# Performance work log

Measured on AMD Instinct MI355X. Metric: run time of the kernel, lower is better.

Reference implementation:

```python
import jax, jax.numpy as jnp
import numpy as np

N, E, D, ATT = 20000, 5000, 128, 32
NUM_LAYERS = 4
LN_EPS = 1e-5
DEG_EPS = 1e-12

def setup_inputs() -> dict:
    key = jax.random.key(0)
    k1, k2, k3, k4 = jax.random.split(key, 4)
    node_embeddings = jax.random.normal(k1, (N, D), dtype=jnp.float32)
    hypergraph_matrix = (jax.random.uniform(k2, (N, E)) < 0.01).astype(jnp.float32)
    ln_gamma = jnp.ones((D,), jnp.float32)
    ln_beta = jnp.zeros((D,), jnp.float32)
    W_att = jax.random.normal(k3, (D, ATT), dtype=jnp.float32) * (1.0 / np.sqrt(D))
    b_att = jnp.zeros((ATT,), jnp.float32)
    q_att = jax.random.normal(k4, (ATT,), dtype=jnp.float32)
    return {"node_embeddings": node_embeddings, "hypergraph_matrix": hypergraph_matrix,
            "ln_gamma": ln_gamma, "ln_beta": ln_beta,
            "W_att": W_att, "b_att": b_att, "q_att": q_att}

def _layernorm(y, gamma, beta):
    mu = jnp.mean(y, axis=-1, keepdims=True)
    var = jnp.mean(jnp.square(y - mu), axis=-1, keepdims=True)
    return (y - mu) * jax.lax.rsqrt(var + LN_EPS) * gamma + beta

def reference(node_embeddings, hypergraph_matrix, ln_gamma, ln_beta, W_att, b_att, q_att):
    H = hypergraph_matrix                      # [N, E]
    dv_inv = 1.0 / jnp.maximum(jnp.sum(H, axis=1), DEG_EPS)   # [N]
    de_inv = 1.0 / jnp.maximum(jnp.sum(H, axis=0), DEG_EPS)   # [E]
    x = node_embeddings
    for _ in range(NUM_LAYERS):
        edge_mean = (H.T @ x) * de_inv[:, None]       # V->E mean, [E, D]
        node_msg = (H @ edge_mean) * dv_inv[:, None]  # E->V mean, [N, D]
        x = _layernorm(node_msg + node_embeddings, ln_gamma, ln_beta)
        # dropout(p=0.35) is identity in eval mode
    # per-edge masked mean over member nodes (vectorized segment-mean)
    M = (H > 0).astype(x.dtype)                        # [N, E]
    cnt = jnp.maximum(jnp.sum(M, axis=0), 1.0)         # [E]
    edge_out = (M.T @ x) / cnt[:, None]                # [E, D]
    # dot-product attention pooling over hyperedges
    scores = jax.nn.softmax(jnp.tanh(edge_out @ W_att + b_att) @ q_att)  # [E]
    return scores @ edge_out                           # [D]
```

## Files before the change

kernel.cpp:

```cpp
#include <hip/hip_runtime.h>
#include <hip/hip_fp16.h>
#include <math.h>

#define NN 20000
#define EE 5000
#define DD 128
#define ATT 32
#define NUM_LAYERS 4
#define LN_EPS 1e-5f
#define DEG_EPS 1e-12f

#define ECAP 320
#define NCAP 128
#define CSTRIDE 32

typedef float vfloat4 __attribute__((ext_vector_type(4)));

__device__ inline unsigned pack2h(float x, float y) {
    return __builtin_bit_cast(unsigned, __floats2half2_rn(x, y));
}
__device__ inline void acc8(float* a, uint4 u) {
    __half2 h;
    h = __builtin_bit_cast(__half2, u.x); a[0] += __low2float(h); a[1] += __high2float(h);
    h = __builtin_bit_cast(__half2, u.y); a[2] += __low2float(h); a[3] += __high2float(h);
    h = __builtin_bit_cast(__half2, u.z); a[4] += __low2float(h); a[5] += __high2float(h);
    h = __builtin_bit_cast(__half2, u.w); a[6] += __low2float(h); a[7] += __high2float(h);
}

__global__ __launch_bounds__(256) void build_adj(
    const float* __restrict__ H, int* __restrict__ cur, int* __restrict__ nc,
    int* __restrict__ el, int* __restrict__ nl) {
    const int n = blockIdx.x;
    const int tid = threadIdx.x;
    __shared__ int lcnt;
    __shared__ int lbuf[NCAP];
    if (tid == 0) lcnt = 0;
    __syncthreads();
    const vfloat4* row = reinterpret_cast<const vfloat4*>(H + (size_t)n * EE);
    for (int i = tid; i < EE / 4; i += 256) {
        const vfloat4 h = __builtin_nontemporal_load(row + i);
        float v[4] = {h.x, h.y, h.z, h.w};
        const int ebase = i * 4;
#pragma unroll
        for (int k = 0; k < 4; k++) {
            if (v[k] != 0.0f) {
                int s = atomicAdd(&lcnt, 1);
                if (s < NCAP) lbuf[s] = ebase + k;
            }
        }
    }
    __syncthreads();
    const int c = min(lcnt, NCAP);
    for (int k = tid; k < c; k += 256) {
        const int e = lbuf[k];
        nl[(size_t)n * NCAP + k] = e;
        const int slot = atomicAdd(&cur[e << 5], 1);
        if (slot < ECAP) el[(size_t)e * ECAP + slot] = n;
    }
    if (tid == 0) nc[n] = lcnt;
}

__global__ __launch_bounds__(256) void cvt_to_h(
    const float* __restrict__ src, __half* __restrict__ dst, int n4) {
    const int i = blockIdx.x * 256 + threadIdx.x;
    if (i >= n4) return;
    const float4 v = reinterpret_cast<const float4*>(src)[i];
    uint2 u; u.x = pack2h(v.x, v.y); u.y = pack2h(v.z, v.w);
    reinterpret_cast<uint2*>(dst)[i] = u;
}

template <bool FINAL>
__global__ __launch_bounds__(256) void edge_gather16(
    const __half* __restrict__ xh, const int* __restrict__ cur,
    const int* __restrict__ el, __half* __restrict__ outh,
    float* __restrict__ eout, const float* __restrict__ W,
    const float* __restrict__ bb, const float* __restrict__ qv,
    float* __restrict__ t) {
    __shared__ int ilst[ECAP];
    __shared__ float part[4][16][8];
    __shared__ float rowbuf[DD];
    const int e = blockIdx.x;
    const int tid = threadIdx.x;
    const int cnt = cur[e << 5];
    const int c = min(cnt, ECAP);
    const int* lst = el + (size_t)e * ECAP;
    for (int k = tid; k < c; k += 256) ilst[k] = lst[k];
    __syncthreads();
    const int lane16 = tid & 15;
    const int s = tid >> 4;
    const int wave = tid >> 6;
    float a[8] = {0, 0, 0, 0, 0, 0, 0, 0};
    float b[8] = {0, 0, 0, 0, 0, 0, 0, 0};
    int i = s;
    for (; i + 16 < c; i += 32) {
        const int n0 = ilst[i];
        const int n1 = ilst[i + 16];
        acc8(a, *reinterpret_cast<const uint4*>(xh + n0 * DD + lane16 * 8));
        acc8(b, *reinterpret_cast<const uint4*>(xh + n1 * DD + lane16 * 8));
    }
    if (i < c) {
        acc8(a, *reinterpret_cast<const uint4*>(xh + ilst[i] * DD + lane16 * 8));
    }
#pragma unroll
    for (int k = 0; k < 8; k++) {
        float v = a[k] + b[k];
        v += __shfl_down(v, 16);
        v += __shfl_down(v, 32);
        a[k] = v;
    }
    if ((tid & 63) < 16) {
#pragma unroll
        for (int k = 0; k < 8; k++) part[wave][lane16][k] = a[k];
    }
    __syncthreads();
    if (tid < 16) {
        const float inv = 1.0f / fmaxf((float)cnt, DEG_EPS);
        float o[8];
#pragma unroll
        for (int k = 0; k < 8; k++)
            o[k] = (part[0][tid][k] + part[1][tid][k] + part[2][tid][k] + part[3][tid][k]) * inv;
        if (!FINAL) {
            uint4 u;
            u.x = pack2h(o[0], o[1]); u.y = pack2h(o[2], o[3]);
            u.z = pack2h(o[4], o[5]); u.w = pack2h(o[6], o[7]);
            *reinterpret_cast<uint4*>(outh + e * DD + tid * 8) = u;
        } else {
#pragma unroll
            for (int k = 0; k < 8; k++) rowbuf[tid * 8 + k] = o[k];
            *reinterpret_cast<float4*>(eout + e * DD + tid * 8) =
                make_float4(o[0], o[1], o[2], o[3]);
            *reinterpret_cast<float4*>(eout + e * DD + tid * 8 + 4) =
                make_float4(o[4], o[5], o[6], o[7]);
        }
    }
    if (FINAL) {
        __syncthreads();
        float r = 0.0f;
        if (tid < ATT) {
            float acc = 0.0f;
#pragma unroll 4
            for (int d = 0; d < DD; d++) acc += rowbuf[d] * W[d * ATT + tid];
            r = tanhf(acc + bb[tid]) * qv[tid];
        }
        for (int off = 16; off > 0; off >>= 1) r += __shfl_down(r, off);
        if (tid == 0) t[e] = r;
    }
}

__global__ __launch_bounds__(128) void node_gather_ln16(
    const __half* __restrict__ emean, const int* __restrict__ nc,
    const int* __restrict__ nl, const float* __restrict__ x0,
    const float* __restrict__ gamma, const float* __restrict__ beta,
    __half* __restrict__ xout) {
    __shared__ int ilst[NCAP];
    __shared__ float part[2][16][8];
    const int n = blockIdx.x;
    const int tid = threadIdx.x;
    const int cnt = nc[n];
    const int c = min(cnt, NCAP);
    const int* lst = nl + (size_t)n * NCAP;
    if (tid < c) ilst[tid] = lst[tid];
    __syncthreads();
    const int lane16 = tid & 15;
    const int s = tid >> 4;
    const int wave = tid >> 6;
    float a[8] = {0, 0, 0, 0, 0, 0, 0, 0};
    float b[8] = {0, 0, 0, 0, 0, 0, 0, 0};
    int i = s;
    for (; i + 8 < c; i += 16) {
        const int e0 = ilst[i];
        const int e1 = ilst[i + 8];
        acc8(a, *reinterpret_cast<const uint4*>(emean + e0 * DD + lane16 * 8));
        acc8(b, *reinterpret_cast<const uint4*>(emean + e1 * DD + lane16 * 8));
    }
    if (i < c) {
        acc8(a, *reinterpret_cast<const uint4*>(emean + ilst[i] * DD + lane16 * 8));
    }
#pragma unroll
    for (int k = 0; k < 8; k++) {
        float v = a[k] + b[k];
        v += __shfl_down(v, 16);
        v += __shfl_down(v, 32);
        a[k] = v;
    }
    if ((tid & 63) < 16) {
#pragma unroll
        for (int k = 0; k < 8; k++) part[wave][lane16][k] = a[k];
    }
    __syncthreads();
    if (tid < 16) {
        const float inv = 1.0f / fmaxf((float)cnt, DEG_EPS);
        const float4 x0a = *reinterpret_cast<const float4*>(x0 + n * DD + tid * 8);
        const float4 x0b = *reinterpret_cast<const float4*>(x0 + n * DD + tid * 8 + 4);
        float y[8];
        y[0] = (part[0][tid][0] + part[1][tid][0]) * inv + x0a.x;
        y[1] = (part[0][tid][1] + part[1][tid][1]) * inv + x0a.y;
        y[2] = (part[0][tid][2] + part[1][tid][2]) * inv + x0a.z;
        y[3] = (part[0][tid][3] + part[1][tid][3]) * inv + x0a.w;
        y[4] = (part[0][tid][4] + part[1][tid][4]) * inv + x0b.x;
        y[5] = (part[0][tid][5] + part[1][tid][5]) * inv + x0b.y;
        y[6] = (part[0][tid][6] + part[1][tid][6]) * inv + x0b.z;
        y[7] = (part[0][tid][7] + part[1][tid][7]) * inv + x0b.w;
        float sm = 0.0f, ss = 0.0f;
#pragma unroll
        for (int k = 0; k < 8; k++) { sm += y[k]; ss += y[k] * y[k]; }
        for (int off = 8; off > 0; off >>= 1) {
            sm += __shfl_down(sm, off);
            ss += __shfl_down(ss, off);
        }
        sm = __shfl(sm, 0);
        ss = __shfl(ss, 0);
        const float mu = sm * (1.0f / 128.0f);
        float var = ss * (1.0f / 128.0f) - mu * mu;
        var = fmaxf(var, 0.0f);
        const float rstd = 1.0f / sqrtf(var + LN_EPS);
        const float4 g0 = *reinterpret_cast<const float4*>(gamma + tid * 8);
        const float4 g1 = *reinterpret_cast<const float4*>(gamma + tid * 8 + 4);
        const float4 b0 = *reinterpret_cast<const float4*>(beta + tid * 8);
        const float4 b1 = *reinterpret_cast<const float4*>(beta + tid * 8 + 4);
        float gg[8] = {g0.x, g0.y, g0.z, g0.w, g1.x, g1.y, g1.z, g1.w};
        float bb[8] = {b0.x, b0.y, b0.z, b0.w, b1.x, b1.y, b1.z, b1.w};
        float o[8];
#pragma unroll
        for (int k = 0; k < 8; k++) o[k] = (y[k] - mu) * rstd * gg[k] + bb[k];
        uint4 u;
        u.x = pack2h(o[0], o[1]); u.y = pack2h(o[2], o[3]);
        u.z = pack2h(o[4], o[5]); u.w = pack2h(o[6], o[7]);
        *reinterpret_cast<uint4*>(xout + n * DD + tid * 8) = u;
    }
}

__global__ __launch_bounds__(1024) void softmax_stats(
    const float* __restrict__ t, float* __restrict__ MS) {
    __shared__ float red[16];
    __shared__ float smax;
    const int tid = threadIdx.x;
    const int wid = tid >> 6;
    float m = -1e30f;
    for (int i = tid; i < EE; i += 1024) m = fmaxf(m, t[i]);
    for (int off = 32; off > 0; off >>= 1) m = fmaxf(m, __shfl_down(m, off));
    if ((tid & 63) == 0) red[wid] = m;
    __syncthreads();
    if (tid < 64) {
        float v = (tid < 16) ? red[tid] : -1e30f;
        for (int off = 8; off > 0; off >>= 1) v = fmaxf(v, __shfl_down(v, off));
        if (tid == 0) smax = v;
    }
    __syncthreads();
    const float M = smax;
    float sum = 0.0f;
    for (int i = tid; i < EE; i += 1024) sum += expf(t[i] - M);
    for (int off = 32; off > 0; off >>= 1) sum += __shfl_down(sum, off);
    if ((tid & 63) == 0) red[wid] = sum;
    __syncthreads();
    if (tid < 64) {
        float v = (tid < 16) ? red[tid] : 0.0f;
        for (int off = 8; off > 0; off >>= 1) v += __shfl_down(v, off);
        if (tid == 0) { MS[0] = M; MS[1] = v; }
    }
}

__global__ __launch_bounds__(128) void weighted_sum(
    const float* __restrict__ eout, const float* __restrict__ t,
    const float* __restrict__ MS, float* __restrict__ out) {
    const int d = threadIdx.x;
    const float M = MS[0];
    const float invS = 1.0f / MS[1];
    float acc = 0.0f;
    for (int e = blockIdx.x; e < EE; e += gridDim.x) {
        const float w = expf(t[e] - M);
        acc += w * eout[e * DD + d];
    }
    atomicAdd(&out[d], acc * invS);
}

extern "C" void kernel_launch(void* const* d_in, const int* in_sizes, int n_in,
                              void* d_out, int out_size, void* d_ws, size_t ws_size,
                              hipStream_t stream) {
    const float* x0 = (const float*)d_in[0];
    const float* H = (const float*)d_in[1];
    const float* gamma = (const float*)d_in[2];
    const float* beta = (const float*)d_in[3];
    const float* W = (const float*)d_in[4];
    const float* b = (const float*)d_in[5];
    const float* qv = (const float*)d_in[6];
    float* out = (float*)d_out;

    char* w = (char*)d_ws;
    int* cur = (int*)w;       w += (size_t)EE * CSTRIDE * 4;
    int* nc = (int*)w;        w += (size_t)NN * 4;
    int* el = (int*)w;        w += (size_t)EE * ECAP * 4;
    int* nl = (int*)w;        w += (size_t)NN * NCAP * 4;
    __half* xh0 = (__half*)w; w += (size_t)NN * DD * 2;
    __half* xA = (__half*)w;  w += (size_t)NN * DD * 2;
    __half* xB = (__half*)w;  w += (size_t)NN * DD * 2;
    __half* emean = (__half*)w; w += (size_t)EE * DD * 2;
    float* eout = (float*)w;  w += (size_t)EE * DD * 4;
    float* t = (float*)w;     w += (size_t)EE * 4;
    float* MS = (float*)w;    w += 16;

    hipMemsetAsync(cur, 0, (size_t)EE * CSTRIDE * 4, stream);
    hipMemsetAsync(d_out, 0, (size_t)DD * sizeof(float), stream);

    build_adj<<<NN, 256, 0, stream>>>(H, cur, nc, el, nl);
    cvt_to_h<<<(NN * DD / 4 + 255) / 256, 256, 0, stream>>>(x0, xh0, NN * DD / 4);

    const __half* xin = xh0;
    __half* bufs[2] = {xA, xB};
    for (int l = 0; l < NUM_LAYERS; l++) {
        edge_gather16<false><<<EE, 256, 0, stream>>>(
            xin, cur, el, emean, nullptr, nullptr, nullptr, nullptr, nullptr);
        node_gather_ln16<<<NN, 128, 0, stream>>>(
            emean, nc, nl, x0, gamma, beta, bufs[l & 1]);
        xin = bufs[l & 1];
    }

    edge_gather16<true><<<EE, 256, 0, stream>>>(
        xin, cur, el, nullptr, eout, W, b, qv, t);
    softmax_stats<<<1, 1024, 0, stream>>>(t, MS);
    weighted_sum<<<64, 128, 0, stream>>>(eout, t, MS, out);
}
```

Baseline: 757.4 us.

## Fuse fp16 conversion into adjacency build, unroll gathers, widen weighted_sum grid

Folds the fp32-to-fp16 conversion of the node embeddings into build_adj, so one kernel launch goes away. Adds a 4-way unrolled gather loop to the edge and node gather kernels, issuing more independent 16-byte loads before accumulating to raise memory-level parallelism. Raises the weighted_sum grid from 64 to 256 blocks. The runtime is dominated by the H scan in build_adj, so the gains are probably small, and the extra loads raise register pressure.

```diff
diff --git a/kernel.cpp b/kernel.cpp
--- a/kernel.cpp
+++ b/kernel.cpp
@@ -29,7 +29,8 @@
 
 __global__ __launch_bounds__(256) void build_adj(
     const float* __restrict__ H, int* __restrict__ cur, int* __restrict__ nc,
-    int* __restrict__ el, int* __restrict__ nl) {
+    int* __restrict__ el, int* __restrict__ nl,
+    const float* __restrict__ x0, __half* __restrict__ xh0) {
     const int n = blockIdx.x;
     const int tid = threadIdx.x;
     __shared__ int lcnt;
@@ -57,16 +58,11 @@
         const int slot = atomicAdd(&cur[e << 5], 1);
         if (slot < ECAP) el[(size_t)e * ECAP + slot] = n;
     }
+    if (tid < 64) {
+        const float2 v = reinterpret_cast<const float2*>(x0 + (size_t)n * DD)[tid];
+        reinterpret_cast<unsigned*>(xh0 + (size_t)n * DD)[tid] = pack2h(v.x, v.y);
+    }
     if (tid == 0) nc[n] = lcnt;
-}
-
-__global__ __launch_bounds__(256) void cvt_to_h(
-    const float* __restrict__ src, __half* __restrict__ dst, int n4) {
-    const int i = blockIdx.x * 256 + threadIdx.x;
-    if (i >= n4) return;
-    const float4 v = reinterpret_cast<const float4*>(src)[i];
-    uint2 u; u.x = pack2h(v.x, v.y); u.y = pack2h(v.z, v.w);
-    reinterpret_cast<uint2*>(dst)[i] = u;
 }
 
 template <bool FINAL>
@@ -92,11 +88,23 @@
     float a[8] = {0, 0, 0, 0, 0, 0, 0, 0};
     float b[8] = {0, 0, 0, 0, 0, 0, 0, 0};
     int i = s;
+    for (; i + 48 < c; i += 64) {
+        const int n0 = ilst[i];
+        const int n1 = ilst[i + 16];
+        const int n2 = ilst[i + 32];
+        const int n3 = ilst[i + 48];
+        const uint4 u0 = *reinterpret_cast<const uint4*>(xh + n0 * DD + lane16 * 8);
+        const uint4 u1 = *reinterpret_cast<const uint4*>(xh + n1 * DD + lane16 * 8);
+        const uint4 u2 = *reinterpret_cast<const uint4*>(xh + n2 * DD + lane16 * 8);
+        const uint4 u3 = *reinterpret_cast<const uint4*>(xh + n3 * DD + lane16 * 8);
+        acc8(a, u0); acc8(b, u1); acc8(a, u2); acc8(b, u3);
+    }
     for (; i + 16 < c; i += 32) {
         const int n0 = ilst[i];
         const int n1 = ilst[i + 16];
-        acc8(a, *reinterpret_cast<const uint4*>(xh + n0 * DD + lane16 * 8));
-        acc8(b, *reinterpret_cast<const uint4*>(xh + n1 * DD + lane16 * 8));
+        const uint4 u0 = *reinterpret_cast<const uint4*>(xh + n0 * DD + lane16 * 8);
+        const uint4 u1 = *reinterpret_cast<const uint4*>(xh + n1 * DD + lane16 * 8);
+        acc8(a, u0); acc8(b, u1);
     }
     if (i < c) {
         acc8(a, *reinterpret_cast<const uint4*>(xh + ilst[i] * DD + lane16 * 8));
@@ -167,11 +175,23 @@
     float a[8] = {0, 0, 0, 0, 0, 0, 0, 0};
     float b[8] = {0, 0, 0, 0, 0, 0, 0, 0};
     int i = s;
+    for (; i + 24 < c; i += 32) {
+        const int e0 = ilst[i];
+        const int e1 = ilst[i + 8];
+        const int e2 = ilst[i + 16];
+        const int e3 = ilst[i + 24];
+        const uint4 u0 = *reinterpret_cast<const uint4*>(emean + e0 * DD + lane16 * 8);
+        const uint4 u1 = *reinterpret_cast<const uint4*>(emean + e1 * DD + lane16 * 8);
+        const uint4 u2 = *reinterpret_cast<const uint4*>(emean + e2 * DD + lane16 * 8);
+        const uint4 u3 = *reinterpret_cast<const uint4*>(emean + e3 * DD + lane16 * 8);
+        acc8(a, u0); acc8(b, u1); acc8(a, u2); acc8(b, u3);
+    }
     for (; i + 8 < c; i += 16) {
         const int e0 = ilst[i];
         const int e1 = ilst[i + 8];
-        acc8(a, *reinterpret_cast<const uint4*>(emean + e0 * DD + lane16 * 8));
-        acc8(b, *reinterpret_cast<const uint4*>(emean + e1 * DD + lane16 * 8));
+        const uint4 u0 = *reinterpret_cast<const uint4*>(emean + e0 * DD + lane16 * 8);
+        const uint4 u1 = *reinterpret_cast<const uint4*>(emean + e1 * DD + lane16 * 8);
+        acc8(a, u0); acc8(b, u1);
     }
     if (i < c) {
         acc8(a, *reinterpret_cast<const uint4*>(emean + ilst[i] * DD + lane16 * 8));
@@ -302,8 +322,7 @@
     hipMemsetAsync(cur, 0, (size_t)EE * CSTRIDE * 4, stream);
     hipMemsetAsync(d_out, 0, (size_t)DD * sizeof(float), stream);
 
-    build_adj<<<NN, 256, 0, stream>>>(H, cur, nc, el, nl);
-    cvt_to_h<<<(NN * DD / 4 + 255) / 256, 256, 0, stream>>>(x0, xh0, NN * DD / 4);
+    build_adj<<<NN, 256, 0, stream>>>(H, cur, nc, el, nl, x0, xh0);
 
     const __half* xin = xh0;
     __half* bufs[2] = {xA, xB};
@@ -318,5 +337,5 @@
     edge_gather16<true><<<EE, 256, 0, stream>>>(
         xin, cur, el, nullptr, eout, W, b, qv, t);
     softmax_stats<<<1, 1024, 0, stream>>>(t, MS);
-    weighted_sum<<<64, 128, 0, stream>>>(eout, t, MS, out);
-}
+    weighted_sum<<<256, 128, 0, stream>>>(eout, t, MS, out);
+}
```

Result: faster. 730.6 us (-3.5%).

## Replace sparse gather aggregation with bit-packed dense MFMA GEMMs

Applied to the files above, without the earlier changes.

Replaces the adjacency-list gather kernels with dense matrix products. The incidence matrix is packed into bitmasks in both orientations, and each bitmask byte is expanded through a shared-memory lookup table into fp16 ones and zeros that feed fp16 MFMA instructions. Node features are kept transposed in fp16. The edge GEMM splits K eight ways and accumulates with atomics, and the node GEMM fuses degree scaling and LayerNorm. This trades irregular gather latency for dense compute over a ~1% dense matrix, so about 100x more raw FLOPs are executed in exchange for regular memory access.

```diff
diff --git a/kernel.cpp b/kernel.cpp
--- a/kernel.cpp
+++ b/kernel.cpp
@@ -9,225 +9,302 @@
 #define NUM_LAYERS 4
 #define LN_EPS 1e-5f
 #define DEG_EPS 1e-12f
-
-#define ECAP 320
-#define NCAP 128
 #define CSTRIDE 32
 
-typedef float vfloat4 __attribute__((ext_vector_type(4)));
-
-__device__ inline unsigned pack2h(float x, float y) {
-    return __builtin_bit_cast(unsigned, __floats2half2_rn(x, y));
-}
-__device__ inline void acc8(float* a, uint4 u) {
-    __half2 h;
-    h = __builtin_bit_cast(__half2, u.x); a[0] += __low2float(h); a[1] += __high2float(h);
-    h = __builtin_bit_cast(__half2, u.y); a[2] += __low2float(h); a[3] += __high2float(h);
-    h = __builtin_bit_cast(__half2, u.z); a[4] += __low2float(h); a[5] += __high2float(h);
-    h = __builtin_bit_cast(__half2, u.w); a[6] += __low2float(h); a[7] += __high2float(h);
-}
-
-__global__ __launch_bounds__(256) void build_adj(
-    const float* __restrict__ H, int* __restrict__ cur, int* __restrict__ nc,
-    int* __restrict__ el, int* __restrict__ nl) {
+#define EPAD 5024
+#define CPAD 5056
+#define KE   20480
+#define KN   5120
+#define HnROW 640
+#define HeROW 2560
+
+typedef _Float16 f16;
+typedef f16 f16x8 __attribute__((ext_vector_type(8)));
+typedef float f32x4 __attribute__((ext_vector_type(4)));
+
+__device__ inline f16x8 asf16x8(uint4 u) {
+    union { uint4 u; f16x8 h; } c; c.u = u; return c.h;
+}
+__device__ inline unsigned short h16(float v) {
+    return __half_as_ushort(__float2half_rn(v));
+}
+
+
+__global__ __launch_bounds__(256) void pack_h(
+    const float* __restrict__ H, unsigned* __restrict__ Hn,
+    unsigned* __restrict__ He, int* __restrict__ cur, int* __restrict__ nc) {
     const int n = blockIdx.x;
-    const int tid = threadIdx.x;
-    __shared__ int lcnt;
-    __shared__ int lbuf[NCAP];
-    if (tid == 0) lcnt = 0;
-    __syncthreads();
-    const vfloat4* row = reinterpret_cast<const vfloat4*>(H + (size_t)n * EE);
-    for (int i = tid; i < EE / 4; i += 256) {
-        const vfloat4 h = __builtin_nontemporal_load(row + i);
-        float v[4] = {h.x, h.y, h.z, h.w};
-        const int ebase = i * 4;
-#pragma unroll
-        for (int k = 0; k < 4; k++) {
-            if (v[k] != 0.0f) {
-                int s = atomicAdd(&lcnt, 1);
-                if (s < NCAP) lbuf[s] = ebase + k;
-            }
-        }
-    }
-    __syncthreads();
-    const int c = min(lcnt, NCAP);
-    for (int k = tid; k < c; k += 256) {
-        const int e = lbuf[k];
-        nl[(size_t)n * NCAP + k] = e;
-        const int slot = atomicAdd(&cur[e << 5], 1);
-        if (slot < ECAP) el[(size_t)e * ECAP + slot] = n;
-    }
-    if (tid == 0) nc[n] = lcnt;
-}
-
-__global__ __launch_bounds__(256) void cvt_to_h(
-    const float* __restrict__ src, __half* __restrict__ dst, int n4) {
-    const int i = blockIdx.x * 256 + threadIdx.x;
-    if (i >= n4) return;
-    const float4 v = reinterpret_cast<const float4*>(src)[i];
-    uint2 u; u.x = pack2h(v.x, v.y); u.y = pack2h(v.z, v.w);
-    reinterpret_cast<uint2*>(dst)[i] = u;
-}
-
-template <bool FINAL>
-__global__ __launch_bounds__(256) void edge_gather16(
-    const __half* __restrict__ xh, const int* __restrict__ cur,
-    const int* __restrict__ el, __half* __restrict__ outh,
-    float* __restrict__ eout, const float* __restrict__ W,
+    const int t = threadIdx.x;
+    const int w = t >> 6, l = t & 63;
+    __shared__ int red[4];
+    int cnt = 0;
+    unsigned long long* hnrow =
+        (unsigned long long*)((char*)Hn + (size_t)n * HnROW);
+    const float* hrow = H + (size_t)n * EE;
+    for (int g = w; g < 80; g += 4) {
+        const int e = g * 64 + l;
+        float v = 0.0f;
+        if (e < EE) v = __builtin_nontemporal_load(hrow + e);
+        const bool p = (v != 0.0f);
+        const unsigned long long m = __ballot(p);
+        if (l == 0) { hnrow[g] = m; cnt += (int)__popcll(m); }
+        if (p) {
+            atomicAdd(&cur[e << 5], 1);
+            atomicOr(&He[(size_t)e * (HeROW / 4) + (n >> 5)], 1u << (n & 31));
+        }
+    }
+    if (l == 0) red[w] = cnt;
+    __syncthreads();
+    if (t == 0) nc[n] = red[0] + red[1] + red[2] + red[3];
+}
+
+__global__ __launch_bounds__(256) void xt_build(
+    const float* __restrict__ x0, unsigned char* __restrict__ xTb) {
+    __shared__ unsigned short Lt[64][136];
+    const int n0 = blockIdx.x * 64;
+    const int t = threadIdx.x;
+    const int rr = t >> 2, q = t & 3;
+    const int n = n0 + rr;
+#pragma unroll
+    for (int j = 0; j < 8; j++) {
+        float4 v = make_float4(0.f, 0.f, 0.f, 0.f);
+        if (n < NN) v = *(const float4*)(x0 + (size_t)n * DD + q * 32 + j * 4);
+        Lt[rr][q * 32 + j * 4 + 0] = h16(v.x);
+        Lt[rr][q * 32 + j * 4 + 1] = h16(v.y);
+        Lt[rr][q * 32 + j * 4 + 2] = h16(v.z);
+        Lt[rr][q * 32 + j * 4 + 3] = h16(v.w);
+    }
+    __syncthreads();
+    const int d = t >> 1, half = t & 1;
+    union { unsigned short s[32]; uint4 q4[4]; } u;
+#pragma unroll
+    for (int i = 0; i < 32; i++) u.s[i] = Lt[half * 32 + i][d];
+    uint4* dst = (uint4*)(xTb + (size_t)d * (KE * 2) +
+                          (size_t)(n0 + half * 32) * 2);
+#pragma unroll
+    for (int i = 0; i < 4; i++) dst[i] = u.q4[i];
+}
+
+__global__ __launch_bounds__(256) void gemm_e(
+    const unsigned char* __restrict__ Heb, const unsigned char* __restrict__ xTb,
+    float* __restrict__ Cacc) {
+    __shared__ uint4 lut[256];
+    {
+        const int t = threadIdx.x;
+        unsigned w0 = ((t & 1) ? 0x3C00u : 0u) | ((t & 2) ? 0x3C000000u : 0u);
+        unsigned w1 = ((t & 4) ? 0x3C00u : 0u) | ((t & 8) ? 0x3C000000u : 0u);
+        unsigned w2 = ((t & 16) ? 0x3C00u : 0u) | ((t & 32) ? 0x3C000000u : 0u);
+        unsigned w3 = ((t & 64) ? 0x3C00u : 0u) | ((t & 128) ? 0x3C000000u : 0u);
+        lut[t] = make_uint4(w0, w1, w2, w3);
+    }
+    __syncthreads();
+    const int bid = blockIdx.x;
+    const int mt = bid % 157, kc = bid / 157;
+    const int e0 = mt * 32;
+    const int kbeg = kc * (KE / 8), kend = kbeg + (KE / 8);
+    const int t = threadIdx.x;
+    const int w = t >> 6, l = t & 63;
+    const int lr = l & 15, lk = l >> 4;
+    const int sh = lk * 8;
+    f32x4 a00 = {0,0,0,0}, a01 = {0,0,0,0}, a10 = {0,0,0,0}, a11 = {0,0,0,0};
+    const unsigned char* ar0 = Heb + (size_t)(e0 + lr) * HeROW;
+    const unsigned char* ar1 = Heb + (size_t)(e0 + 16 + lr) * HeROW;
+    const unsigned char* br0 = xTb + (size_t)(w * 32 + lr) * (KE * 2) + lk * 16;
+    const unsigned char* br1 = xTb + (size_t)(w * 32 + 16 + lr) * (KE * 2) + lk * 16;
+    for (int k0 = kbeg; k0 < kend; k0 += 128) {
+        const uint4 bw0 = *(const uint4*)(ar0 + (k0 >> 3));
+        const uint4 bw1 = *(const uint4*)(ar1 + (k0 >> 3));
+        uint4 b0[4], b1[4];
+#pragma unroll
+        for (int t4 = 0; t4 < 4; t4++) {
+            b0[t4] = *(const uint4*)(br0 + (size_t)(k0 + t4 * 32) * 2);
+            b1[t4] = *(const uint4*)(br1 + (size_t)(k0 + t4 * 32) * 2);
+        }
+        const unsigned wa0[4] = {bw0.x, bw0.y, bw0.z, bw0.w};
+        const unsigned wa1[4] = {bw1.x, bw1.y, bw1.z, bw1.w};
+#pragma unroll
+        for (int t4 = 0; t4 < 4; t4++) {
+            const f16x8 fa0 = asf16x8(lut[(wa0[t4] >> sh) & 0xFF]);
+            const f16x8 fa1 = asf16x8(lut[(wa1[t4] >> sh) & 0xFF]);
+            const f16x8 fb0 = asf16x8(b0[t4]);
+            const f16x8 fb1 = asf16x8(b1[t4]);
+            a00 = __builtin_amdgcn_mfma_f32_16x16x32_f16(fa0, fb0, a00, 0, 0, 0);
+            a01 = __builtin_amdgcn_mfma_f32_16x16x32_f16(fa0, fb1, a01, 0, 0, 0);
+            a10 = __builtin_amdgcn_mfma_f32_16x16x32_f16(fa1, fb0, a10, 0, 0, 0);
+            a11 = __builtin_amdgcn_mfma_f32_16x16x32_f16(fa1, fb1, a11, 0, 0, 0);
+        }
+    }
+#pragma unroll
+    for (int r = 0; r < 4; r++) {
+        atomicAdd(&Cacc[(size_t)(e0 + lk * 4 + r) * DD + w * 32 + lr], a00[r]);
+        atomicAdd(&Cacc[(size_t)(e0 + lk * 4 + r) * DD + w * 32 + 16 + lr], a01[r]);
+        atomicAdd(&Cacc[(size_t)(e0 + 16 + lk * 4 + r) * DD + w * 32 + lr], a10[r]);
+        atomicAdd(&Cacc[(size_t)(e0 + 16 + lk * 4 + r) * DD + w * 32 + 16 + lr], a11[r]);
+    }
+}
+
+__global__ __launch_bounds__(256) void ep_edge(
+    float* __restrict__ Cacc, const int* __restrict__ cur,
+    unsigned char* __restrict__ emTb, float* __restrict__ eout,
+    const int isFinal) {
+    __shared__ unsigned short Lt[64][136];
+    const int e0 = blockIdx.x * 64;
+    const int t = threadIdx.x;
+    const int rr = t >> 2, q = t & 3;
+    const int e = e0 + rr;
+    float de = 0.0f;
+    if (e < EE) de = (float)cur[e << 5];
+    const float s = isFinal ? (1.0f / fmaxf(de, 1.0f))
+                            : (1.0f / fmaxf(de, DEG_EPS));
+    float* crow = Cacc + (size_t)e * DD + q * 32;
+#pragma unroll
+    for (int j = 0; j < 8; j++) {
+        float4 v = *(float4*)(crow + j * 4);
+        *(float4*)(crow + j * 4) = make_float4(0.f, 0.f, 0.f, 0.f);
+        v.x *= s; v.y *= s; v.z *= s; v.w *= s;
+        if (isFinal) {
+            if (e < EE)
+                *(float4*)(eout + (size_t)e * DD + q * 32 + j * 4) = v;
+        } else {
+            Lt[rr][q * 32 + j * 4 + 0] = h16(v.x);
+            Lt[rr][q * 32 + j * 4 + 1] = h16(v.y);
+            Lt[rr][q * 32 + j * 4 + 2] = h16(v.z);
+            Lt[rr][q * 32 + j * 4 + 3] = h16(v.w);
+        }
+    }
+    if (!isFinal) {
+        __syncthreads();
+        const int d = t >> 1, half = t & 1;
+        union { unsigned short s[32]; uint4 q4[4]; } u;
+#pragma unroll
+        for (int i = 0; i < 32; i++) u.s[i] = Lt[half * 32 + i][d];
+        uint4* dst = (uint4*)(emTb + (size_t)d * (KN * 2) +
+                              (size_t)(e0 + half * 32) * 2);
+#pragma unroll
+        for (int i = 0; i < 4; i++) dst[i] = u.q4[i];
+    }
+}
+
+__global__ __launch_bounds__(256) void gemm_n(
+    const unsigned char* __restrict__ Hnb, const unsigned char* __restrict__ emTb,
+    const int* __restrict__ nc, const float* __restrict__ x0,
+    const float* __restrict__ gamma, const float* __restrict__ beta,
+    unsigned char* __restrict__ xTb) {
+    __shared__ uint4 lut[256];
+    __shared__ float Csm[32][132];
+    __shared__ unsigned short Lt[32][136];
+    {
+        const int t = threadIdx.x;
+        unsigned w0 = ((t & 1) ? 0x3C00u : 0u) | ((t & 2) ? 0x3C000000u : 0u);
+        unsigned w1 = ((t & 4) ? 0x3C00u : 0u) | ((t & 8) ? 0x3C000000u : 0u);
+        unsigned w2 = ((t & 16) ? 0x3C00u : 0u) | ((t & 32) ? 0x3C000000u : 0u);
+        unsigned w3 = ((t & 64) ? 0x3C00u : 0u) | ((t & 128) ? 0x3C000000u : 0u);
+        lut[t] = make_uint4(w0, w1, w2, w3);
+    }
+    __syncthreads();
+    const int n0 = blockIdx.x * 32;
+    const int t = threadIdx.x;
+    const int w = t >> 6, l = t & 63;
+    const int lr = l & 15, lk = l >> 4;
+    const int sh = lk * 8;
+    f32x4 a00 = {0,0,0,0}, a01 = {0,0,0,0}, a10 = {0,0,0,0}, a11 = {0,0,0,0};
+    const unsigned char* ar0 = Hnb + (size_t)(n0 + lr) * HnROW;
+    const unsigned char* ar1 = Hnb + (size_t)(n0 + 16 + lr) * HnROW;
+    const unsigned char* br0 = emTb + (size_t)(w * 32 + lr) * (KN * 2) + lk * 16;
+    const unsigned char* br1 = emTb + (size_t)(w * 32 + 16 + lr) * (KN * 2) + lk * 16;
+    for (int k0 = 0; k0 < KN; k0 += 128) {
+        const uint4 bw0 = *(const uint4*)(ar0 + (k0 >> 3));
+        const uint4 bw1 = *(const uint4*)(ar1 + (k0 >> 3));
+        uint4 b0[4], b1[4];
+#pragma unroll
+        for (int t4 = 0; t4 < 4; t4++) {
+            b0[t4] = *(const uint4*)(br0 + (size_t)(k0 + t4 * 32) * 2);
+            b1[t4] = *(const uint4*)(br1 + (size_t)(k0 + t4 * 32) * 2);
+        }
+        const unsigned wa0[4] = {bw0.x, bw0.y, bw0.z, bw0.w};
+        const unsigned wa1[4] = {bw1.x, bw1.y, bw1.z, bw1.w};
+#pragma unroll
+        for (int t4 = 0; t4 < 4; t4++) {
+            const f16x8 fa0 = asf16x8(lut[(wa0[t4] >> sh) & 0xFF]);
+            const f16x8 fa1 = asf16x8(lut[(wa1[t4] >> sh) & 0xFF]);
+            const f16x8 fb0 = asf16x8(b0[t4]);
+            const f16x8 fb1 = asf16x8(b1[t4]);
+            a00 = __builtin_amdgcn_mfma_f32_16x16x32_f16(fa0, fb0, a00, 0, 0, 0);
+            a01 = __builtin_amdgcn_mfma_f32_16x16x32_f16(fa0, fb1, a01, 0, 0, 0);
+            a10 = __builtin_amdgcn_mfma_f32_16x16x32_f16(fa1, fb0, a10, 0, 0, 0);
+            a11 = __builtin_amdgcn_mfma_f32_16x16x32_f16(fa1, fb1, a11, 0, 0, 0);
+        }
+    }
+#pragma unroll
+    for (int r = 0; r < 4; r++) {
+        Csm[lk * 4 + r][w * 32 + lr] = a00[r];
+        Csm[lk * 4 + r][w * 32 + 16 + lr] = a01[r];
+        Csm[16 + lk * 4 + r][w * 32 + lr] = a10[r];
+        Csm[16 + lk * 4 + r][w * 32 + 16 + lr] = a11[r];
+    }
+    __syncthreads();
+    const int rr = t >> 3, q = t & 7;
+    const int n = n0 + rr;
+    const float dvinv = 1.0f / fmaxf((float)nc[n], DEG_EPS);
+    float y[16];
+    float sm = 0.0f, ss = 0.0f;
+#pragma unroll
+    for (int j = 0; j < 4; j++) {
+        const float4 xr = *(const float4*)(x0 + (size_t)n * DD + q * 16 + j * 4);
+        float v0 = Csm[rr][q * 16 + j * 4 + 0] * dvinv + xr.x;
+        float v1 = Csm[rr][q * 16 + j * 4 + 1] * dvinv + xr.y;
+        float v2 = Csm[rr][q * 16 + j * 4 + 2] * dvinv + xr.z;
+        float v3 = Csm[rr][q * 16 + j * 4 + 3] * dvinv + xr.w;
+        y[j * 4 + 0] = v0; y[j * 4 + 1] = v1; y[j * 4 + 2] = v2; y[j * 4 + 3] = v3;
+        sm += v0 + v1 + v2 + v3;
+        ss += v0 * v0 + v1 * v1 + v2 * v2 + v3 * v3;
+    }
+    sm += __shfl_xor(sm, 1); sm += __shfl_xor(sm, 2); sm += __shfl_xor(sm, 4);
+    ss += __shfl_xor(ss, 1); ss += __shfl_xor(ss, 2); ss += __shfl_xor(ss, 4);
+    const float mu = sm * (1.0f / 128.0f);
+    float var = ss * (1.0f / 128.0f) - mu * mu;
+    var = fmaxf(var, 0.0f);
+    const float rstd = 1.0f / sqrtf(var + LN_EPS);
+#pragma unroll
+    for (int j = 0; j < 4; j++) {
+        const float4 g = *(const float4*)(gamma + q * 16 + j * 4);
+        const float4 bb = *(const float4*)(beta + q * 16 + j * 4);
+        Lt[rr][q * 16 + j * 4 + 0] = h16((y[j * 4 + 0] - mu) * rstd * g.x + bb.x);
+        Lt[rr][q * 16 + j * 4 + 1] = h16((y[j * 4 + 1] - mu) * rstd * g.y + bb.y);
+        Lt[rr][q * 16 + j * 4 + 2] = h16((y[j * 4 + 2] - mu) * rstd * g.z + bb.z);
+        Lt[rr][q * 16 + j * 4 + 3] = h16((y[j * 4 + 3] - mu) * rstd * g.w + bb.w);
+    }
+    __syncthreads();
+    const int d = t >> 1, half = t & 1;
+    union { unsigned short s[16]; uint4 q4[2]; } u;
+#pragma unroll
+    for (int i = 0; i < 16; i++) u.s[i] = Lt[half * 16 + i][d];
+    uint4* dst = (uint4*)(xTb + (size_t)d * (KE * 2) +
+                          (size_t)(n0 + half * 16) * 2);
+    dst[0] = u.q4[0];
+    dst[1] = u.q4[1];
+}
+
+__global__ __launch_bounds__(64) void logits(
+    const float* __restrict__ eout, const float* __restrict__ W,
     const float* __restrict__ bb, const float* __restrict__ qv,
     float* __restrict__ t) {
-    __shared__ int ilst[ECAP];
-    __shared__ float part[4][16][8];
     __shared__ float rowbuf[DD];
     const int e = blockIdx.x;
     const int tid = threadIdx.x;
-    const int cnt = cur[e << 5];
-    const int c = min(cnt, ECAP);
-    const int* lst = el + (size_t)e * ECAP;
-    for (int k = tid; k < c; k += 256) ilst[k] = lst[k];
-    __syncthreads();
-    const int lane16 = tid & 15;
-    const int s = tid >> 4;
-    const int wave = tid >> 6;
-    float a[8] = {0, 0, 0, 0, 0, 0, 0, 0};
-    float b[8] = {0, 0, 0, 0, 0, 0, 0, 0};
-    int i = s;
-    for (; i + 16 < c; i += 32) {
-        const int n0 = ilst[i];
-        const int n1 = ilst[i + 16];
-        acc8(a, *reinterpret_cast<const uint4*>(xh + n0 * DD + lane16 * 8));
-        acc8(b, *reinterpret_cast<const uint4*>(xh + n1 * DD + lane16 * 8));
-    }
-    if (i < c) {
-        acc8(a, *reinterpret_cast<const uint4*>(xh + ilst[i] * DD + lane16 * 8));
-    }
-#pragma unroll
-    for (int k = 0; k < 8; k++) {
-        float v = a[k] + b[k];
-        v += __shfl_down(v, 16);
-        v += __shfl_down(v, 32);
-        a[k] = v;
-    }
-    if ((tid & 63) < 16) {
-#pragma unroll
-        for (int k = 0; k < 8; k++) part[wave][lane16][k] = a[k];
-    }
-    __syncthreads();
-    if (tid < 16) {
-        const float inv = 1.0f / fmaxf((float)cnt, DEG_EPS);
-        float o[8];
-#pragma unroll
-        for (int k = 0; k < 8; k++)
-            o[k] = (part[0][tid][k] + part[1][tid][k] + part[2][tid][k] + part[3][tid][k]) * inv;
-        if (!FINAL) {
-            uint4 u;
-            u.x = pack2h(o[0], o[1]); u.y = pack2h(o[2], o[3]);
-            u.z = pack2h(o[4], o[5]); u.w = pack2h(o[6], o[7]);
-            *reinterpret_cast<uint4*>(outh + e * DD + tid * 8) = u;
-        } else {
-#pragma unroll
-            for (int k = 0; k < 8; k++) rowbuf[tid * 8 + k] = o[k];
-            *reinterpret_cast<float4*>(eout + e * DD + tid * 8) =
-                make_float4(o[0], o[1], o[2], o[3]);
-            *reinterpret_cast<float4*>(eout + e * DD + tid * 8 + 4) =
-                make_float4(o[4], o[5], o[6], o[7]);
-        }
-    }
-    if (FINAL) {
-        __syncthreads();
-        float r = 0.0f;
-        if (tid < ATT) {
-            float acc = 0.0f;
+    const float2 v = reinterpret_cast<const float2*>(eout + (size_t)e * DD)[tid];
+    rowbuf[tid * 2] = v.x;
+    rowbuf[tid * 2 + 1] = v.y;
+    __syncthreads();
+    float r = 0.0f;
+    if (tid < ATT) {
+        float acc = 0.0f;
 #pragma unroll 4
-            for (int d = 0; d < DD; d++) acc += rowbuf[d] * W[d * ATT + tid];
-            r = tanhf(acc + bb[tid]) * qv[tid];
-        }
-        for (int off = 16; off > 0; off >>= 1) r += __shfl_down(r, off);
-        if (tid == 0) t[e] = r;
-    }
-}
-
-__global__ __launch_bounds__(128) void node_gather_ln16(
-    const __half* __restrict__ emean, const int* __restrict__ nc,
-    const int* __restrict__ nl, const float* __restrict__ x0,
-    const float* __restrict__ gamma, const float* __restrict__ beta,
-    __half* __restrict__ xout) {
-    __shared__ int ilst[NCAP];
-    __shared__ float part[2][16][8];
-    const int n = blockIdx.x;
-    const int tid = threadIdx.x;
-    const int cnt = nc[n];
-    const int c = min(cnt, NCAP);
-    const int* lst = nl + (size_t)n * NCAP;
-    if (tid < c) ilst[tid] = lst[tid];
-    __syncthreads();
-    const int lane16 = tid & 15;
-    const int s = tid >> 4;
-    const int wave = tid >> 6;
-    float a[8] = {0, 0, 0, 0, 0, 0, 0, 0};
-    float b[8] = {0, 0, 0, 0, 0, 0, 0, 0};
-    int i = s;
-    for (; i + 8 < c; i += 16) {
-        const int e0 = ilst[i];
-        const int e1 = ilst[i + 8];
-        acc8(a, *reinterpret_cast<const uint4*>(emean + e0 * DD + lane16 * 8));
-        acc8(b, *reinterpret_cast<const uint4*>(emean + e1 * DD + lane16 * 8));
-    }
-    if (i < c) {
-        acc8(a, *reinterpret_cast<const uint4*>(emean + ilst[i] * DD + lane16 * 8));
-    }
-#pragma unroll
-    for (int k = 0; k < 8; k++) {
-        float v = a[k] + b[k];
-        v += __shfl_down(v, 16);
-        v += __shfl_down(v, 32);
-        a[k] = v;
-    }
-    if ((tid & 63) < 16) {
-#pragma unroll
-        for (int k = 0; k < 8; k++) part[wave][lane16][k] = a[k];
-    }
-    __syncthreads();
-    if (tid < 16) {
-        const float inv = 1.0f / fmaxf((float)cnt, DEG_EPS);
-        const float4 x0a = *reinterpret_cast<const float4*>(x0 + n * DD + tid * 8);
-        const float4 x0b = *reinterpret_cast<const float4*>(x0 + n * DD + tid * 8 + 4);
-        float y[8];
-        y[0] = (part[0][tid][0] + part[1][tid][0]) * inv + x0a.x;
-        y[1] = (part[0][tid][1] + part[1][tid][1]) * inv + x0a.y;
-        y[2] = (part[0][tid][2] + part[1][tid][2]) * inv + x0a.z;
-        y[3] = (part[0][tid][3] + part[1][tid][3]) * inv + x0a.w;
-        y[4] = (part[0][tid][4] + part[1][tid][4]) * inv + x0b.x;
-        y[5] = (part[0][tid][5] + part[1][tid][5]) * inv + x0b.y;
-        y[6] = (part[0][tid][6] + part[1][tid][6]) * inv + x0b.z;
-        y[7] = (part[0][tid][7] + part[1][tid][7]) * inv + x0b.w;
-        float sm = 0.0f, ss = 0.0f;
-#pragma unroll
-        for (int k = 0; k < 8; k++) { sm += y[k]; ss += y[k] * y[k]; }
-        for (int off = 8; off > 0; off >>= 1) {
-            sm += __shfl_down(sm, off);
-            ss += __shfl_down(ss, off);
-        }
-        sm = __shfl(sm, 0);
-        ss = __shfl(ss, 0);
-        const float mu = sm * (1.0f / 128.0f);
-        float var = ss * (1.0f / 128.0f) - mu * mu;
-        var = fmaxf(var, 0.0f);
-        const float rstd = 1.0f / sqrtf(var + LN_EPS);
-        const float4 g0 = *reinterpret_cast<const float4*>(gamma + tid * 8);
-        const float4 g1 = *reinterpret_cast<const float4*>(gamma + tid * 8 + 4);
-        const float4 b0 = *reinterpret_cast<const float4*>(beta + tid * 8);
-        const float4 b1 = *reinterpret_cast<const float4*>(beta + tid * 8 + 4);
-        float gg[8] = {g0.x, g0.y, g0.z, g0.w, g1.x, g1.y, g1.z, g1.w};
-        float bb[8] = {b0.x, b0.y, b0.z, b0.w, b1.x, b1.y, b1.z, b1.w};
-        float o[8];
-#pragma unroll
-        for (int k = 0; k < 8; k++) o[k] = (y[k] - mu) * rstd * gg[k] + bb[k];
-        uint4 u;
-        u.x = pack2h(o[0], o[1]); u.y = pack2h(o[2], o[3]);
-        u.z = pack2h(o[4], o[5]); u.w = pack2h(o[6], o[7]);
-        *reinterpret_cast<uint4*>(xout + n * DD + tid * 8) = u;
-    }
+        for (int d = 0; d < DD; d++) acc += rowbuf[d] * W[d * ATT + tid];
+        r = tanhf(acc + bb[tid]) * qv[tid];
+    }
+    for (int off = 16; off > 0; off >>= 1) r += __shfl_down(r, off);
+    if (tid == 0) t[e] = r;
 }
 
 __global__ __launch_bounds__(1024) void softmax_stats(
@@ -286,37 +363,40 @@
     const float* qv = (const float*)d_in[6];
     float* out = (float*)d_out;
 
-    char* w = (char*)d_ws;
-    int* cur = (int*)w;       w += (size_t)EE * CSTRIDE * 4;
-    int* nc = (int*)w;        w += (size_t)NN * 4;
-    int* el = (int*)w;        w += (size_t)EE * ECAP * 4;
-    int* nl = (int*)w;        w += (size_t)NN * NCAP * 4;
-    __half* xh0 = (__half*)w; w += (size_t)NN * DD * 2;
-    __half* xA = (__half*)w;  w += (size_t)NN * DD * 2;
-    __half* xB = (__half*)w;  w += (size_t)NN * DD * 2;
-    __half* emean = (__half*)w; w += (size_t)EE * DD * 2;
-    float* eout = (float*)w;  w += (size_t)EE * DD * 4;
-    float* t = (float*)w;     w += (size_t)EE * 4;
-    float* MS = (float*)w;    w += 16;
-
-    hipMemsetAsync(cur, 0, (size_t)EE * CSTRIDE * 4, stream);
+    size_t off = 0;
+    auto alloc = [&](size_t bytes) -> char* {
+        char* p = (char*)d_ws + off;
+        off += (bytes + 255) & ~(size_t)255;
+        return p;
+    };
+    int* cur = (int*)alloc((size_t)EE * CSTRIDE * 4);
+    unsigned char* Heb = (unsigned char*)alloc((size_t)EPAD * HeROW);
+    float* Cacc = (float*)alloc((size_t)CPAD * DD * 4);
+    unsigned char* xTb = (unsigned char*)alloc((size_t)DD * KE * 2);
+    unsigned char* emTb = (unsigned char*)alloc((size_t)DD * KN * 2);
+    const size_t zend = off;
+    unsigned char* Hnb = (unsigned char*)alloc((size_t)NN * HnROW);
+    int* nc = (int*)alloc((size_t)NN * 4);
+    float* eout = (float*)alloc((size_t)EE * DD * 4);
+    float* tt = (float*)alloc((size_t)EE * 4);
+    float* MS = (float*)alloc(64);
+    (void)ws_size;
+
+    hipMemsetAsync(d_ws, 0, zend, stream);
     hipMemsetAsync(d_out, 0, (size_t)DD * sizeof(float), stream);
 
-    build_adj<<<NN, 256, 0, stream>>>(H, cur, nc, el, nl);
-    cvt_to_h<<<(NN * DD / 4 + 255) / 256, 256, 0, stream>>>(x0, xh0, NN * DD / 4);
-
-    const __half* xin = xh0;
-    __half* bufs[2] = {xA, xB};
+    pack_h<<<NN, 256, 0, stream>>>(H, (unsigned*)Hnb, (unsigned*)Heb, cur, nc);
+    xt_build<<<313, 256, 0, stream>>>(x0, xTb);
+
     for (int l = 0; l < NUM_LAYERS; l++) {
-        edge_gather16<false><<<EE, 256, 0, stream>>>(
-            xin, cur, el, emean, nullptr, nullptr, nullptr, nullptr, nullptr);
-        node_gather_ln16<<<NN, 128, 0, stream>>>(
-            emean, nc, nl, x0, gamma, beta, bufs[l & 1]);
-        xin = bufs[l & 1];
-    }
-
-    edge_gather16<true><<<EE, 256, 0, stream>>>(
-        xin, cur, el, nullptr, eout, W, b, qv, t);
-    softmax_stats<<<1, 1024, 0, stream>>>(t, MS);
-    weighted_sum<<<64, 128, 0, stream>>>(eout, t, MS, out);
-}
+        gemm_e<<<157 * 8, 256, 0, stream>>>(Heb, xTb, Cacc);
+        ep_edge<<<79, 256, 0, stream>>>(Cacc, cur, emTb, nullptr, 0);
+        gemm_n<<<625, 256, 0, stream>>>(Hnb, emTb, nc, x0, gamma, beta, xTb);
+    }
+
+    gemm_e<<<157 * 8, 256, 0, stream>>>(Heb, xTb, Cacc);
+    ep_edge<<<79, 256, 0, stream>>>(Cacc, cur, nullptr, eout, 1);
+    logits<<<EE, 64, 0, stream>>>(eout, W, b, qv, tt);
+    softmax_stats<<<1, 1024, 0, stream>>>(tt, MS);
+    weighted_sum<<<256, 128, 0, stream>>>(eout, tt, MS, out);
+}
```

New measurement: 1.780 ms. 135% more time.
